# Optimization experiments

Hardware: AMD Instinct MI355X
Metric: run time of the kernel (lower is better)

## Reference

```python
import jax, jax.numpy as jnp
import numpy as np

EPS = 1e-8

def setup_inputs() -> dict:
    key = jax.random.key(0)
    k1, k2, k3 = jax.random.split(key, 3)
    B, A = 4, 2048
    positions = jax.random.normal(k1, (B, A, 3), dtype=jnp.float32)
    neighbors = jax.random.randint(k2, (B, A, A), 0, A, dtype=jnp.int64)
    neighbor_mask = jax.random.randint(k3, (B, A), 0, 2).astype(bool)
    return {"positions": positions, "neighbors": neighbors, "neighbor_mask": neighbor_mask}

def _safe_norm(dist_vec):
    # torch.norm has zero (sub)gradient at 0; guard sqrt for jax parity
    d2 = jnp.sum(dist_vec * dist_vec, axis=-1)  # [B, A, N]
    safe = jnp.sqrt(jnp.where(d2 > 0, d2, 1.0))
    return jnp.where(d2 > 0, safe, 0.0)

def reference(positions, neighbors, neighbor_mask):
    B, A, _ = positions.shape
    # gather neighbor positions: pos_xyz[b, i, j] = positions[b, neighbors[b, i, j]]
    pos_xyz = positions[jnp.arange(B)[:, None, None], neighbors]  # [B, A, N, 3]
    dist_vec = pos_xyz - positions[:, :, None, :]                  # [B, A, N, 3]
    distances = _safe_norm(dist_vec)                               # [B, A, N]
    distances = 1.0 / (distances + EPS)
    # pairwise mask = outer product of per-atom mask (requires N == A)
    mask2 = neighbor_mask[:, :, None] & neighbor_mask[:, None, :]  # [B, A, A]
    eye = jnp.eye(A, dtype=bool)[None]
    distances = jnp.where(eye, 0.0, distances)   # zero diagonal
    distances = jnp.where(mask2, distances, 0.0)  # mask out invalid pairs
    return distances
```

## Files before the change

### kernel.cpp

```cpp
#include <hip/hip_runtime.h>


constexpr int A_DIM = 2048;
constexpr int WPB   = 8;
constexpr int NTHR  = WPB * 64;

__global__ __launch_bounds__(NTHR, 8) void atom_distances_kernel(
    const float* __restrict__ pos,
    const int*   __restrict__ nbr,
    const int*   __restrict__ mask,
    float*       __restrict__ out) {
  __shared__ float    sxyz[3 * A_DIM];
  __shared__ unsigned smaskbits[A_DIM / 32];

  const int blocks_per_b = A_DIM / WPB;
  const int b  = blockIdx.x / blocks_per_b;
  const int i0 = (blockIdx.x % blocks_per_b) * WPB;

  const float* posb  = pos  + (size_t)b * A_DIM * 3;
  const int*   maskb = mask + (size_t)b * A_DIM;

  for (int t = threadIdx.x; t < A_DIM; t += NTHR) {
    sxyz[t]             = posb[3 * t + 0];
    sxyz[t + A_DIM]     = posb[3 * t + 1];
    sxyz[t + 2 * A_DIM] = posb[3 * t + 2];
  }
  for (int r = 0; r < A_DIM / NTHR; ++r) {
    const int t = r * NTHR + threadIdx.x;
    const unsigned long long bal = __ballot(maskb[t] != 0);
    if ((threadIdx.x & 63) == 0) {
      const int wbase = t >> 5;
      smaskbits[wbase]     = (unsigned)bal;
      smaskbits[wbase + 1] = (unsigned)(bal >> 32);
    }
  }
  __syncthreads();

  const int w    = threadIdx.x >> 6;
  const int lane = threadIdx.x & 63;
  const int i    = i0 + w;

  float* orow = out + ((size_t)b * A_DIM + i) * A_DIM;

  const unsigned mi = (smaskbits[i >> 5] >> (i & 31)) & 1u;

  if (mi == 0) {
    const float4 z = make_float4(0.f, 0.f, 0.f, 0.f);
    #pragma unroll
    for (int c = 0; c < A_DIM / (64 * 4); ++c) {
      const int j0 = (c * 64 + lane) * 4;
      *reinterpret_cast<float4*>(orow + j0) = z;
    }
    return;
  }

  const float pix = sxyz[i];
  const float piy = sxyz[i + A_DIM];
  const float piz = sxyz[i + 2 * A_DIM];

  const int* nrow = nbr + ((size_t)b * A_DIM + i) * A_DIM;

  #pragma unroll 2
  for (int c = 0; c < A_DIM / (64 * 4); ++c) {
    const int j0 = (c * 64 + lane) * 4;
    const int4 n = *reinterpret_cast<const int4*>(nrow + j0);

    const unsigned wbits = smaskbits[c * 8 + (lane >> 3)];
    const int bit = (lane & 7) * 4;

    float4 r;
    {
      const int t = n.x & (A_DIM - 1);
      const float dx = sxyz[t] - pix, dy = sxyz[t + A_DIM] - piy, dz = sxyz[t + 2 * A_DIM] - piz;
      const float d  = __builtin_amdgcn_sqrtf(dx * dx + dy * dy + dz * dz);
      const float m  = (float)((wbits >> (bit + 0)) & 1u) * ((i != j0 + 0) ? 1.0f : 0.0f);
      r.x = m * __builtin_amdgcn_rcpf(d + 1e-8f);
    }
    {
      const int t = n.y & (A_DIM - 1);
      const float dx = sxyz[t] - pix, dy = sxyz[t + A_DIM] - piy, dz = sxyz[t + 2 * A_DIM] - piz;
      const float d  = __builtin_amdgcn_sqrtf(dx * dx + dy * dy + dz * dz);
      const float m  = (float)((wbits >> (bit + 1)) & 1u) * ((i != j0 + 1) ? 1.0f : 0.0f);
      r.y = m * __builtin_amdgcn_rcpf(d + 1e-8f);
    }
    {
      const int t = n.z & (A_DIM - 1);
      const float dx = sxyz[t] - pix, dy = sxyz[t + A_DIM] - piy, dz = sxyz[t + 2 * A_DIM] - piz;
      const float d  = __builtin_amdgcn_sqrtf(dx * dx + dy * dy + dz * dz);
      const float m  = (float)((wbits >> (bit + 2)) & 1u) * ((i != j0 + 2) ? 1.0f : 0.0f);
      r.z = m * __builtin_amdgcn_rcpf(d + 1e-8f);
    }
    {
      const int t = n.w & (A_DIM - 1);
      const float dx = sxyz[t] - pix, dy = sxyz[t + A_DIM] - piy, dz = sxyz[t + 2 * A_DIM] - piz;
      const float d  = __builtin_amdgcn_sqrtf(dx * dx + dy * dy + dz * dz);
      const float m  = (float)((wbits >> (bit + 3)) & 1u) * ((i != j0 + 3) ? 1.0f : 0.0f);
      r.w = m * __builtin_amdgcn_rcpf(d + 1e-8f);
    }

    *reinterpret_cast<float4*>(orow + j0) = r;
  }
}

extern "C" void kernel_launch(void* const* d_in, const int* in_sizes, int n_in,
                              void* d_out, int out_size, void* d_ws, size_t ws_size,
                              hipStream_t stream) {
  const float* pos  = (const float*)d_in[0];
  const int*   nbr  = (const int*)d_in[1];
  const int*   mask = (const int*)d_in[2];
  float*       out  = (float*)d_out;

  const int B = in_sizes[2] / A_DIM;
  const int grid = B * (A_DIM / WPB);

  atom_distances_kernel<<<grid, NTHR, 0, stream>>>(pos, nbr, mask, out);
}
```

Measured before the change: 24.46 us.

## Prefetch neighbor indices, use nontemporal stores, and replace sqrt+rcp with rsq

Output stores, including the zero-fill path for masked rows, become nontemporal so the write-only output stream does not occupy cache. The neighbor-index loads are software-pipelined four chunks ahead through explicit registers, so more global loads are in flight per wave. The sqrt plus reciprocal pair becomes a single rsq with a guard for zero distance, and the mask multiply becomes a select. This raises register pressure, and rsq drops the 1e-8 epsilon, which slightly changes results for very small distances.

```diff
diff --git a/kernel.cpp b/kernel.cpp
--- a/kernel.cpp
+++ b/kernel.cpp
@@ -1,5 +1,7 @@
 #include <hip/hip_runtime.h>
 
+
+typedef float f4 __attribute__((ext_vector_type(4)));
 
 constexpr int A_DIM = 2048;
 constexpr int WPB   = 8;
@@ -41,16 +43,13 @@
   const int i    = i0 + w;
 
   float* orow = out + ((size_t)b * A_DIM + i) * A_DIM;
-
   const unsigned mi = (smaskbits[i >> 5] >> (i & 31)) & 1u;
 
   if (mi == 0) {
-    const float4 z = make_float4(0.f, 0.f, 0.f, 0.f);
+    const f4 z = {0.f, 0.f, 0.f, 0.f};
     #pragma unroll
-    for (int c = 0; c < A_DIM / (64 * 4); ++c) {
-      const int j0 = (c * 64 + lane) * 4;
-      *reinterpret_cast<float4*>(orow + j0) = z;
-    }
+    for (int c = 0; c < 8; ++c)
+      __builtin_nontemporal_store(z, reinterpret_cast<f4*>(orow + (c * 64 + lane) * 4));
     return;
   }
 
@@ -60,46 +59,41 @@
 
   const int* nrow = nbr + ((size_t)b * A_DIM + i) * A_DIM;
 
-  #pragma unroll 2
-  for (int c = 0; c < A_DIM / (64 * 4); ++c) {
-    const int j0 = (c * 64 + lane) * 4;
-    const int4 n = *reinterpret_cast<const int4*>(nrow + j0);
+#define LDN(c) (*reinterpret_cast<const int4*>(nrow + ((c) * 64 + lane) * 4))
 
-    const unsigned wbits = smaskbits[c * 8 + (lane >> 3)];
-    const int bit = (lane & 7) * 4;
+#define ELEM(nt_, e_, dst_) { \
+    const int t_ = (nt_) & (A_DIM - 1); \
+    const float dx_ = sxyz[t_] - pix; \
+    const float dy_ = sxyz[t_ + A_DIM] - piy; \
+    const float dz_ = sxyz[t_ + 2 * A_DIM] - piz; \
+    const float d2_ = dx_ * dx_ + dy_ * dy_ + dz_ * dz_; \
+    const float inv_ = d2_ > 0.0f ? __builtin_amdgcn_rsqf(d2_) : 1e8f; \
+    dst_ = ((((wbits >> (bit + e_)) & 1u) != 0u) & (i != j0 + e_)) ? inv_ : 0.0f; }
 
-    float4 r;
-    {
-      const int t = n.x & (A_DIM - 1);
-      const float dx = sxyz[t] - pix, dy = sxyz[t + A_DIM] - piy, dz = sxyz[t + 2 * A_DIM] - piz;
-      const float d  = __builtin_amdgcn_sqrtf(dx * dx + dy * dy + dz * dz);
-      const float m  = (float)((wbits >> (bit + 0)) & 1u) * ((i != j0 + 0) ? 1.0f : 0.0f);
-      r.x = m * __builtin_amdgcn_rcpf(d + 1e-8f);
-    }
-    {
-      const int t = n.y & (A_DIM - 1);
-      const float dx = sxyz[t] - pix, dy = sxyz[t + A_DIM] - piy, dz = sxyz[t + 2 * A_DIM] - piz;
-      const float d  = __builtin_amdgcn_sqrtf(dx * dx + dy * dy + dz * dz);
-      const float m  = (float)((wbits >> (bit + 1)) & 1u) * ((i != j0 + 1) ? 1.0f : 0.0f);
-      r.y = m * __builtin_amdgcn_rcpf(d + 1e-8f);
-    }
-    {
-      const int t = n.z & (A_DIM - 1);
-      const float dx = sxyz[t] - pix, dy = sxyz[t + A_DIM] - piy, dz = sxyz[t + 2 * A_DIM] - piz;
-      const float d  = __builtin_amdgcn_sqrtf(dx * dx + dy * dy + dz * dz);
-      const float m  = (float)((wbits >> (bit + 2)) & 1u) * ((i != j0 + 2) ? 1.0f : 0.0f);
-      r.z = m * __builtin_amdgcn_rcpf(d + 1e-8f);
-    }
-    {
-      const int t = n.w & (A_DIM - 1);
-      const float dx = sxyz[t] - pix, dy = sxyz[t + A_DIM] - piy, dz = sxyz[t + 2 * A_DIM] - piz;
-      const float d  = __builtin_amdgcn_sqrtf(dx * dx + dy * dy + dz * dz);
-      const float m  = (float)((wbits >> (bit + 3)) & 1u) * ((i != j0 + 3) ? 1.0f : 0.0f);
-      r.w = m * __builtin_amdgcn_rcpf(d + 1e-8f);
-    }
+#define PROC(c, n) { \
+    const int j0 = ((c) * 64 + lane) * 4; \
+    const unsigned wbits = smaskbits[(c) * 8 + (lane >> 3)]; \
+    const int bit = (lane & 7) * 4; \
+    f4 r; \
+    ELEM(n.x, 0, r.x); \
+    ELEM(n.y, 1, r.y); \
+    ELEM(n.z, 2, r.z); \
+    ELEM(n.w, 3, r.w); \
+    __builtin_nontemporal_store(r, reinterpret_cast<f4*>(orow + j0)); }
 
-    *reinterpret_cast<float4*>(orow + j0) = r;
-  }
+  int4 n0 = LDN(0), n1 = LDN(1), n2 = LDN(2), n3 = LDN(3);
+  PROC(0, n0); n0 = LDN(4);
+  PROC(1, n1); n1 = LDN(5);
+  PROC(2, n2); n2 = LDN(6);
+  PROC(3, n3); n3 = LDN(7);
+  PROC(4, n0);
+  PROC(5, n1);
+  PROC(6, n2);
+  PROC(7, n3);
+
+#undef PROC
+#undef ELEM
+#undef LDN
 }
 
 extern "C" void kernel_launch(void* const* d_in, const int* in_sizes, int n_in,
```

New measurement: 22.54 us. -7.9%, faster.
